# Optimization experiments

Hardware: AMD Instinct MI355X
Metric: run time of the kernel (lower is better)

The kernel has to match this reference:

```python
import jax, jax.numpy as jnp
import numpy as np

N, D1, D2 = 2048, 512, 512

def setup_inputs() -> dict:
    key = jax.random.key(0)
    k1, k2, k3 = jax.random.split(key, 3)
    x = jax.random.normal(k1, (N, D1), dtype=jnp.float32)
    # parameters are drawn N(0, 0.01) in the torch module
    U = 0.01 * jax.random.normal(k2, (N, D1, D2), dtype=jnp.float32)
    bias = 0.01 * jax.random.normal(k3, (N, 1, D2), dtype=jnp.float32)
    return {"x": x, "U": U, "bias": bias}

def reference(x, U, bias):
    # per-sample GEMV: (N,D1) x (N,D1,D2) -> (N,D2), fused bias add
    act = jnp.einsum('nd,nde->ne', x, U)  # bmm of (N,1,D1)@(N,D1,D2) squeezed
    return act + bias[:, 0, :]
```

## Files before the change

### kernel.cpp

```cpp
#include <hip/hip_runtime.h>


constexpr int N  = 2048;
constexpr int D1 = 512;
constexpr int D2 = 512;

__global__ __launch_bounds__(128) void baens_gemv_kernel(
    const float* __restrict__ x,
    const float* __restrict__ U,
    const float* __restrict__ bias,
    float* __restrict__ out)
{
    __shared__ float xs[D1];

    const int n = blockIdx.x;
    const int t = threadIdx.x;

    const float4* xg = reinterpret_cast<const float4*>(x + (size_t)n * D1);
    reinterpret_cast<float4*>(xs)[t] = xg[t];
    __syncthreads();

    const float4* Urow =
        reinterpret_cast<const float4*>(U + (size_t)n * D1 * D2) + t;

    float4 acc = make_float4(0.f, 0.f, 0.f, 0.f);

    #pragma unroll 8
    for (int d = 0; d < D1; ++d) {
        const float xv = xs[d];
        const float4 u = Urow[(size_t)d * (D2 / 4)];
        acc.x += xv * u.x;
        acc.y += xv * u.y;
        acc.z += xv * u.z;
        acc.w += xv * u.w;
    }

    const float4 b =
        reinterpret_cast<const float4*>(bias + (size_t)n * D2)[t];
    float4 o;
    o.x = acc.x + b.x;
    o.y = acc.y + b.y;
    o.z = acc.z + b.z;
    o.w = acc.w + b.w;
    reinterpret_cast<float4*>(out + (size_t)n * D2)[t] = o;
}

extern "C" void kernel_launch(void* const* d_in, const int* in_sizes, int n_in,
                              void* d_out, int out_size, void* d_ws, size_t ws_size,
                              hipStream_t stream) {
    const float* x    = (const float*)d_in[0];
    const float* U    = (const float*)d_in[1];
    const float* bias = (const float*)d_in[2];
    float* out        = (float*)d_out;

    baens_gemv_kernel<<<N, 128, 0, stream>>>(x, U, bias, out);
}
```

Baseline: 2.625 ms.

## Split D1 reduction across eight row groups with shared-memory tree reduction

Each block now uses 1024 threads instead of 128. The threads are arranged as 8 row groups that each cover a strided slice of D1, and the partial float4 sums are combined through a shared-memory tree reduction before the bias add. The aim is many more outstanding global loads per CU, to hide HBM latency in this bandwidth-bound per-sample GEMV. The cost is extra shared memory, three block-wide barriers, and fewer concurrent blocks per CU.

```diff
diff --git a/kernel.cpp b/kernel.cpp
--- a/kernel.cpp
+++ b/kernel.cpp
@@ -5,44 +5,74 @@
 constexpr int D1 = 512;
 constexpr int D2 = 512;
 
-__global__ __launch_bounds__(128) void baens_gemv_kernel(
+constexpr int THREADS = 1024;
+constexpr int CQ = D2 / 4;
+constexpr int RS = THREADS / CQ;
+
+__global__ __launch_bounds__(THREADS) void baens_gemv_kernel(
     const float* __restrict__ x,
     const float* __restrict__ U,
     const float* __restrict__ bias,
     float* __restrict__ out)
 {
-    __shared__ float xs[D1];
+    __shared__ float  xs[D1];
+    __shared__ float4 red[RS][CQ];
 
     const int n = blockIdx.x;
     const int t = threadIdx.x;
+    const int c = t & (CQ - 1);
+    const int r = t >> 7;
 
-    const float4* xg = reinterpret_cast<const float4*>(x + (size_t)n * D1);
-    reinterpret_cast<float4*>(xs)[t] = xg[t];
+    if (t < CQ) {
+        reinterpret_cast<float4*>(xs)[t] =
+            reinterpret_cast<const float4*>(x + (size_t)n * D1)[t];
+    }
     __syncthreads();
 
-    const float4* Urow =
-        reinterpret_cast<const float4*>(U + (size_t)n * D1 * D2) + t;
+    const float4* Up =
+        reinterpret_cast<const float4*>(U + (size_t)n * D1 * D2) +
+        (size_t)r * CQ + c;
 
     float4 acc = make_float4(0.f, 0.f, 0.f, 0.f);
 
     #pragma unroll 8
-    for (int d = 0; d < D1; ++d) {
-        const float xv = xs[d];
-        const float4 u = Urow[(size_t)d * (D2 / 4)];
+    for (int i = 0; i < D1 / RS; ++i) {
+        const float xv = xs[i * RS + r];
+        const float4 u = Up[(size_t)i * (RS * CQ)];
         acc.x += xv * u.x;
         acc.y += xv * u.y;
         acc.z += xv * u.z;
         acc.w += xv * u.w;
     }
 
-    const float4 b =
-        reinterpret_cast<const float4*>(bias + (size_t)n * D2)[t];
-    float4 o;
-    o.x = acc.x + b.x;
-    o.y = acc.y + b.y;
-    o.z = acc.z + b.z;
-    o.w = acc.w + b.w;
-    reinterpret_cast<float4*>(out + (size_t)n * D2)[t] = o;
+    red[r][c] = acc;
+    __syncthreads();
+    if (r < 4) {
+        float4 a = red[r][c];
+        const float4 b = red[r + 4][c];
+        a.x += b.x; a.y += b.y; a.z += b.z; a.w += b.w;
+        red[r][c] = a;
+    }
+    __syncthreads();
+    if (r < 2) {
+        float4 a = red[r][c];
+        const float4 b = red[r + 2][c];
+        a.x += b.x; a.y += b.y; a.z += b.z; a.w += b.w;
+        red[r][c] = a;
+    }
+    __syncthreads();
+    if (r == 0) {
+        const float4 a = red[0][c];
+        const float4 b = red[1][c];
+        const float4 bi =
+            reinterpret_cast<const float4*>(bias + (size_t)n * D2)[c];
+        float4 o;
+        o.x = a.x + b.x + bi.x;
+        o.y = a.y + b.y + bi.y;
+        o.z = a.z + b.z + bi.z;
+        o.w = a.w + b.w + bi.w;
+        reinterpret_cast<float4*>(out + (size_t)n * D2)[c] = o;
+    }
 }
 
 extern "C" void kernel_launch(void* const* d_in, const int* in_sizes, int n_in,
@@ -53,5 +83,5 @@
     const float* bias = (const float*)d_in[2];
     float* out        = (float*)d_out;
 
-    baens_gemv_kernel<<<N, 128, 0, stream>>>(x, U, bias, out);
+    baens_gemv_kernel<<<N, THREADS, 0, stream>>>(x, U, bias, out);
 }
```

Result: no change. 2.600 ms (-0.9%).
